# Optimization experiments

Hardware: AMD Instinct MI355X
Metric: run time of the kernel (lower is better)

## Reference

```python
import jax, jax.numpy as jnp
import numpy as np

TH1 = 1.0  # thresholds[0]
TH2 = 1.0  # thresholds[1]

B, IN, H, OUT = 256, 1024, 2048, 1024


def setup_inputs() -> dict:
    key = jax.random.key(0)
    ks = jax.random.split(key, 7)
    # Linear weights scaled like torch default init (~1/sqrt(fan_in)) so spikes occur
    W1 = jax.random.normal(ks[0], (H, IN), jnp.float32) / np.sqrt(IN)
    b1 = jax.random.normal(ks[1], (H,), jnp.float32) * 0.01
    W2 = jax.random.normal(ks[2], (H, H), jnp.float32) / np.sqrt(H)
    b2 = jax.random.normal(ks[3], (H,), jnp.float32) * 0.01
    W3 = jax.random.normal(ks[4], (OUT, H), jnp.float32) / np.sqrt(H)
    b3 = jax.random.normal(ks[5], (OUT,), jnp.float32) * 0.01
    x = jax.random.normal(ks[6], (B, IN), jnp.float32)
    return {"x": x, "W1": W1, "b1": b1, "W2": W2, "b2": b2, "W3": W3, "b3": b3, "T": 50}


def reference(x, W1, b1, W2, b2, W3, b3, T):
    b = x.shape[0]
    dt = x.dtype
    # fc1(x) is identical every timestep; compute once (same math as torch loop)
    i1 = x @ W1.T + b1  # [b, H]

    def step(carry, _):
        v1, v2, v3 = carry
        v1 = v1 + i1
        s1 = (v1 >= TH1).astype(dt)
        v1 = v1 * (1.0 - s1)          # reset on spike
        v2 = v2 + s1 @ W2.T + b2
        s2 = (v2 >= TH2).astype(dt)
        v2 = v2 * (1.0 - s2)
        v3 = v3 + s2 @ W3.T + b3
        return (v1, v2, v3), None

    init = (jnp.zeros((b, W1.shape[0]), dt),
            jnp.zeros((b, W2.shape[0]), dt),
            jnp.zeros((b, W3.shape[0]), dt))
    (v1, v2, v3), _ = jax.lax.scan(step, init, None, length=T)
    return v3 / T
```

## Files before the change

kernel.cpp:

```cpp
#include <hip/hip_runtime.h>

#define NB     256
#define IN1    1024
#define H1     2048
#define OUT3   1024
#define TSTEPS 50
#define KSPLIT 8
#define KSPL3  8

#define QS   (0.15f / 127.f)
#define QS2  (QS / 254.f)

typedef __attribute__((ext_vector_type(4))) int int32x4;

__device__ __forceinline__ void gl2lds16(const void* g, void* l) {
  __builtin_amdgcn_global_load_lds(
      (const __attribute__((address_space(1))) unsigned char*)g,
      (__attribute__((address_space(3))) unsigned char*)l, 16, 0, 0);
}

__global__ __launch_bounds__(256)
void quant_kernel(const float* __restrict__ W, signed char* __restrict__ hi,
                  signed char* __restrict__ lo, int n) {
  int i = blockIdx.x * 256 + threadIdx.x;
  if (i < n) {
    float w = W[i];
    float h = rintf(w * (1.f / QS));
    h = fminf(fmaxf(h, -127.f), 127.f);
    float r = w - h * QS;
    float l2 = fminf(fmaxf(rintf(r * (1.f / QS2)), -127.f), 127.f);
    hi[i] = (signed char)h;
    lo[i] = (signed char)l2;
  }
}

__global__ __launch_bounds__(256)
void sgemm_splitk(const float* __restrict__ A, const float* __restrict__ B,
                  float* __restrict__ P, int M, int N, int K) {
  __shared__ float As[16][68];
  __shared__ float Bs[16][68];
  const int t  = threadIdx.x;
  const int tx = t & 15, ty = t >> 4;
  const int m0 = blockIdx.y * 64, n0 = blockIdx.x * 64;
  const int Kc = K / KSPLIT;
  const int kbeg = blockIdx.z * Kc, kend = kbeg + Kc;
  const int lr = t >> 4, lk = t & 15;
  float acc[4][4] = {};
  for (int k0 = kbeg; k0 < kend; k0 += 16) {
    #pragma unroll
    for (int i = 0; i < 4; ++i) {
      As[lk][lr + i * 16] = A[(size_t)(m0 + lr + i * 16) * K + k0 + lk];
      Bs[lk][lr + i * 16] = B[(size_t)(n0 + lr + i * 16) * K + k0 + lk];
    }
    __syncthreads();
    #pragma unroll
    for (int kk = 0; kk < 16; ++kk) {
      float4 a4 = *(const float4*)&As[kk][ty * 4];
      float4 b4 = *(const float4*)&Bs[kk][tx * 4];
      float av[4] = {a4.x, a4.y, a4.z, a4.w};
      float bv[4] = {b4.x, b4.y, b4.z, b4.w};
      #pragma unroll
      for (int i = 0; i < 4; ++i)
        #pragma unroll
        for (int j = 0; j < 4; ++j)
          acc[i][j] += av[i] * bv[j];
    }
    __syncthreads();
  }
  float* Pp = P + (size_t)blockIdx.z * M * N;
  #pragma unroll
  for (int i = 0; i < 4; ++i)
    #pragma unroll
    for (int j = 0; j < 4; ++j)
      Pp[(size_t)(m0 + ty * 4 + i) * N + n0 + tx * 4 + j] = acc[i][j];
}

__global__ __launch_bounds__(256)
void sim1_kernel(const float* __restrict__ P, const float* __restrict__ b1,
                 signed char* __restrict__ s1all) {
  int idx = blockIdx.x * 256 + threadIdx.x;
  float inp = b1[idx & (H1 - 1)];
  #pragma unroll
  for (int s = 0; s < KSPLIT; ++s) inp += P[(size_t)s * (NB * H1) + idx];
  float v = 0.f;
  #pragma unroll
  for (int t = 0; t < TSTEPS; ++t) {
    v += inp;
    bool s = (v >= 1.0f);
    s1all[(size_t)t * (NB * H1) + idx] = s ? (signed char)1 : (signed char)0;
    if (s) v = 0.f;
  }
}

__global__ __launch_bounds__(256)
void sim2_kernel(const float* __restrict__ A2, const float* __restrict__ b2,
                 float* __restrict__ v2s, float* __restrict__ cnt,
                 signed char* __restrict__ cnt8,
                 int tch, int init, int fin) {
  int idx = blockIdx.x * 256 + threadIdx.x;
  float v = init ? 0.f : v2s[idx];
  float c = init ? 0.f : cnt[idx];
  float bb = b2[idx & (H1 - 1)];
  for (int t = 0; t < tch; ++t) {
    v = v + A2[(size_t)t * (NB * H1) + idx];
    v = v + bb;
    if (v >= 1.0f) { c += 1.f; v = 0.f; }
  }
  if (fin) {
    cnt8[idx] = (signed char)c;
  } else {
    v2s[idx] = v;
    cnt[idx] = c;
  }
}

__global__ __launch_bounds__(256)
void out_epi_kernel(const float* __restrict__ P, const float* __restrict__ b3,
                    float* __restrict__ out) {
  int idx = blockIdx.x * 256 + threadIdx.x;
  float a = 0.f;
  #pragma unroll
  for (int s = 0; s < KSPL3; ++s) a += P[(size_t)s * (NB * OUT3) + idx];
  out[idx] = (a + (float)TSTEPS * b3[idx & (OUT3 - 1)]) * (1.0f / TSTEPS);
}

__global__ __launch_bounds__(512, 4)
void gemm_i8(const signed char* __restrict__ A,
             const signed char* __restrict__ B0,
             const signed char* __restrict__ B1,
             float* __restrict__ C, int M, int N, int K, int Kc) {
  __shared__ signed char As[128 * 128];
  __shared__ signed char Bs[2 * 128 * 128];

  const int gx  = gridDim.x;
  const int nwg = gx * gridDim.y;
  int wg = blockIdx.y * gx + blockIdx.x;
  if (gridDim.z == 1 && (nwg & 7) == 0) wg = (wg & 7) * (nwg >> 3) + (wg >> 3);
  const int bx = wg % gx, by = wg / gx;
  const int m0 = by * 128, n0 = bx * 128;
  const int kbeg = blockIdx.z * Kc, kend = kbeg + Kc;

  const int t  = threadIdx.x;
  const int l  = t & 63;
  const int w  = t >> 6;
  const int wm = w >> 2, wn = w & 3;
  const int lr = l & 15;
  const int lq = l >> 4;
  const int kx = lr & 7;
  const int sr   = t >> 3, c8 = t & 7;
  const int scol = (c8 ^ (sr & 7)) * 16;

  int32x4 acch[4][2], accl[4][2];
  #pragma unroll
  for (int m = 0; m < 4; ++m)
    #pragma unroll
    for (int n = 0; n < 2; ++n) {
      acch[m][n] = (int32x4)(0);
      accl[m][n] = (int32x4)(0);
    }

  #pragma unroll 1
  for (int k0 = kbeg; k0 < kend; k0 += 128) {
    gl2lds16(A  + (size_t)(m0 + sr)      * K + k0 + scol, As + sr * 128 + c8 * 16);
    gl2lds16(A  + (size_t)(m0 + sr + 64) * K + k0 + scol, As + (sr + 64) * 128 + c8 * 16);
    gl2lds16(B0 + (size_t)(n0 + sr)      * K + k0 + scol, Bs + sr * 128 + c8 * 16);
    gl2lds16(B0 + (size_t)(n0 + sr + 64) * K + k0 + scol, Bs + (sr + 64) * 128 + c8 * 16);
    gl2lds16(B1 + (size_t)(n0 + sr)      * K + k0 + scol, Bs + 128 * 128 + sr * 128 + c8 * 16);
    gl2lds16(B1 + (size_t)(n0 + sr + 64) * K + k0 + scol, Bs + 128 * 128 + (sr + 64) * 128 + c8 * 16);
    __syncthreads();

    #pragma unroll
    for (int ks = 0; ks < 2; ++ks) {
      const int kc = ks * 4 + lq;
      const int ko = (kc ^ kx) * 16;
      int32x4 af[4], bf[2];
      #pragma unroll
      for (int m = 0; m < 4; ++m)
        af[m] = *(const int32x4*)(As + (wm * 64 + m * 16 + lr) * 128 + ko);
      #pragma unroll
      for (int n = 0; n < 2; ++n)
        bf[n] = *(const int32x4*)(Bs + (wn * 32 + n * 16 + lr) * 128 + ko);
      #pragma unroll
      for (int m = 0; m < 4; ++m)
        #pragma unroll
        for (int n = 0; n < 2; ++n)
          acch[m][n] = __builtin_amdgcn_mfma_i32_16x16x64_i8(af[m], bf[n], acch[m][n], 0, 0, 0);
      #pragma unroll
      for (int n = 0; n < 2; ++n)
        bf[n] = *(const int32x4*)(Bs + 128 * 128 + (wn * 32 + n * 16 + lr) * 128 + ko);
      #pragma unroll
      for (int m = 0; m < 4; ++m)
        #pragma unroll
        for (int n = 0; n < 2; ++n)
          accl[m][n] = __builtin_amdgcn_mfma_i32_16x16x64_i8(af[m], bf[n], accl[m][n], 0, 0, 0);
    }
    __syncthreads();
  }

  float* Cp = C + (size_t)blockIdx.z * M * N;
  const int crow = lq * 4;
  #pragma unroll
  for (int m = 0; m < 4; ++m) {
    #pragma unroll
    for (int n = 0; n < 2; ++n) {
      int col  = n0 + wn * 32 + n * 16 + lr;
      int rowb = m0 + wm * 64 + m * 16 + crow;
      #pragma unroll
      for (int j = 0; j < 4; ++j)
        Cp[(size_t)(rowb + j) * N + col] =
            QS * (float)acch[m][n][j] + QS2 * (float)accl[m][n][j];
    }
  }
}

extern "C" void kernel_launch(void* const* d_in, const int* in_sizes, int n_in,
                              void* d_out, int out_size, void* d_ws, size_t ws_size,
                              hipStream_t stream) {
  const float* x  = (const float*)d_in[0];
  const float* W1 = (const float*)d_in[1];
  const float* b1 = (const float*)d_in[2];
  const float* W2 = (const float*)d_in[3];
  const float* b2 = (const float*)d_in[4];
  const float* W3 = (const float*)d_in[5];
  const float* b3 = (const float*)d_in[6];
  float* out = (float*)d_out;

  char* ws = (char*)d_ws;
  size_t off = 0;
  auto take = [&](size_t bytes) -> void* {
    void* p = ws + off;
    off += (bytes + 255) & ~(size_t)255;
    return p;
  };
  signed char* W2hi  = (signed char*)take((size_t)H1 * H1);
  signed char* W2lo  = (signed char*)take((size_t)H1 * H1);
  signed char* W3hi  = (signed char*)take((size_t)OUT3 * H1);
  signed char* W3lo  = (signed char*)take((size_t)OUT3 * H1);
  signed char* s1all = (signed char*)take((size_t)TSTEPS * NB * H1);
  float*       v2s   = (float*)take((size_t)NB * H1 * 4);
  float*       cnt   = (float*)take((size_t)NB * H1 * 4);
  signed char* cnt8  = (signed char*)take((size_t)NB * H1);
  size_t part_bytes  = (size_t)KSPLIT * NB * H1 * 4;
  size_t part3_bytes = (size_t)KSPL3 * NB * OUT3 * 4;
  float* Part = (float*)take(part_bytes > part3_bytes ? part_bytes : part3_bytes);

  const size_t plane = (size_t)NB * H1 * 4;
  size_t avail = (ws_size > off) ? (ws_size - off) : 0;
  int CH = (int)(avail / plane);
  if (CH > TSTEPS) CH = TSTEPS;
  if (CH < 1) CH = 1;
  float* A2 = (float*)take((size_t)CH * plane);

  quant_kernel<<<dim3((H1 * H1 + 255) / 256), 256, 0, stream>>>(W2, W2hi, W2lo, H1 * H1);
  quant_kernel<<<dim3((OUT3 * H1 + 255) / 256), 256, 0, stream>>>(W3, W3hi, W3lo, OUT3 * H1);

  sgemm_splitk<<<dim3(H1 / 64, NB / 64, KSPLIT), 256, 0, stream>>>(
      x, W1, Part, NB, H1, IN1);

  sim1_kernel<<<dim3(NB * H1 / 256), 256, 0, stream>>>(Part, b1, s1all);

  for (int c0 = 0; c0 < TSTEPS; c0 += CH) {
    int ch = (TSTEPS - c0 < CH) ? (TSTEPS - c0) : CH;
    gemm_i8<<<dim3(H1 / 128, ch * NB / 128), 512, 0, stream>>>(
        s1all + (size_t)c0 * NB * H1, W2hi, W2lo, A2, ch * NB, H1, H1, H1);
    sim2_kernel<<<dim3(NB * H1 / 256), 256, 0, stream>>>(
        A2, b2, v2s, cnt, cnt8, ch, c0 == 0, c0 + ch >= TSTEPS);
  }

  gemm_i8<<<dim3(OUT3 / 128, NB / 128, KSPL3), 512, 0, stream>>>(
      cnt8, W3hi, W3lo, Part, NB, OUT3, H1, H1 / KSPL3);
  out_epi_kernel<<<dim3(NB * OUT3 / 256), 256, 0, stream>>>(Part, b3, out);
}
```

Before: 170.1 us.

## Double-buffer int8 GEMM LDS tiles and enlarge M tile to 256

The int8 MFMA GEMM now uses a 256x128 output tile and double-buffered LDS staging, so the global-to-LDS loads for the next K slice are issued while MFMAs run on the current one. Explicit waitcnt, sched_barrier and setprio calls are added to overlap LDS fragment reads with the MFMA stream. The aim is to hide load latency and reuse each B tile across more rows. In exchange the kernel needs about 128KB of LDS and more accumulator registers, so occupancy bound drops to 2 and the grid has half as many workgroups, including the small split-K W3 GEMM.

```diff
diff --git a/kernel.cpp b/kernel.cpp
--- a/kernel.cpp
+++ b/kernel.cpp
@@ -124,20 +124,20 @@
   out[idx] = (a + (float)TSTEPS * b3[idx & (OUT3 - 1)]) * (1.0f / TSTEPS);
 }
 
-__global__ __launch_bounds__(512, 4)
+__global__ __launch_bounds__(512, 2)
 void gemm_i8(const signed char* __restrict__ A,
              const signed char* __restrict__ B0,
              const signed char* __restrict__ B1,
              float* __restrict__ C, int M, int N, int K, int Kc) {
-  __shared__ signed char As[128 * 128];
-  __shared__ signed char Bs[2 * 128 * 128];
+  __shared__ signed char As[2][256 * 128];
+  __shared__ signed char Bs[2][2][128 * 128];
 
   const int gx  = gridDim.x;
   const int nwg = gx * gridDim.y;
   int wg = blockIdx.y * gx + blockIdx.x;
   if (gridDim.z == 1 && (nwg & 7) == 0) wg = (wg & 7) * (nwg >> 3) + (wg >> 3);
   const int bx = wg % gx, by = wg / gx;
-  const int m0 = by * 128, n0 = bx * 128;
+  const int m0 = by * 256, n0 = bx * 128;
   const int kbeg = blockIdx.z * Kc, kend = kbeg + Kc;
 
   const int t  = threadIdx.x;
@@ -150,61 +150,90 @@
   const int sr   = t >> 3, c8 = t & 7;
   const int scol = (c8 ^ (sr & 7)) * 16;
 
-  int32x4 acch[4][2], accl[4][2];
-  #pragma unroll
-  for (int m = 0; m < 4; ++m)
+  auto stage = [&](int k0, int b) {
+    #pragma unroll
+    for (int i = 0; i < 4; ++i) {
+      int row = i * 64 + sr;
+      gl2lds16(A + (size_t)(m0 + row) * K + k0 + scol, As[b] + row * 128 + c8 * 16);
+    }
+    #pragma unroll
+    for (int i = 0; i < 2; ++i) {
+      int row = i * 64 + sr;
+      gl2lds16(B0 + (size_t)(n0 + row) * K + k0 + scol, Bs[b][0] + row * 128 + c8 * 16);
+      gl2lds16(B1 + (size_t)(n0 + row) * K + k0 + scol, Bs[b][1] + row * 128 + c8 * 16);
+    }
+  };
+
+  int32x4 acch[8][2], accl[8][2];
+  #pragma unroll
+  for (int m = 0; m < 8; ++m)
     #pragma unroll
     for (int n = 0; n < 2; ++n) {
       acch[m][n] = (int32x4)(0);
       accl[m][n] = (int32x4)(0);
     }
 
+  stage(kbeg, 0);
+  asm volatile("s_waitcnt vmcnt(0)" ::: "memory");
+  __builtin_amdgcn_s_barrier();
+
+  int cur = 0;
   #pragma unroll 1
   for (int k0 = kbeg; k0 < kend; k0 += 128) {
-    gl2lds16(A  + (size_t)(m0 + sr)      * K + k0 + scol, As + sr * 128 + c8 * 16);
-    gl2lds16(A  + (size_t)(m0 + sr + 64) * K + k0 + scol, As + (sr + 64) * 128 + c8 * 16);
-    gl2lds16(B0 + (size_t)(n0 + sr)      * K + k0 + scol, Bs + sr * 128 + c8 * 16);
-    gl2lds16(B0 + (size_t)(n0 + sr + 64) * K + k0 + scol, Bs + (sr + 64) * 128 + c8 * 16);
-    gl2lds16(B1 + (size_t)(n0 + sr)      * K + k0 + scol, Bs + 128 * 128 + sr * 128 + c8 * 16);
-    gl2lds16(B1 + (size_t)(n0 + sr + 64) * K + k0 + scol, Bs + 128 * 128 + (sr + 64) * 128 + c8 * 16);
-    __syncthreads();
+    if (k0 + 128 < kend) stage(k0 + 128, cur ^ 1);
+
+    const signed char* As_ = As[cur];
+    const signed char* Bh_ = Bs[cur][0];
+    const signed char* Bl_ = Bs[cur][1];
 
     #pragma unroll
     for (int ks = 0; ks < 2; ++ks) {
       const int kc = ks * 4 + lq;
       const int ko = (kc ^ kx) * 16;
-      int32x4 af[4], bf[2];
-      #pragma unroll
-      for (int m = 0; m < 4; ++m)
-        af[m] = *(const int32x4*)(As + (wm * 64 + m * 16 + lr) * 128 + ko);
+      int32x4 af[8], bf[2];
+      #pragma unroll
+      for (int m = 0; m < 8; ++m)
+        af[m] = *(const int32x4*)(As_ + (wm * 128 + m * 16 + lr) * 128 + ko);
       #pragma unroll
       for (int n = 0; n < 2; ++n)
-        bf[n] = *(const int32x4*)(Bs + (wn * 32 + n * 16 + lr) * 128 + ko);
-      #pragma unroll
-      for (int m = 0; m < 4; ++m)
+        bf[n] = *(const int32x4*)(Bh_ + (wn * 32 + n * 16 + lr) * 128 + ko);
+      asm volatile("s_waitcnt lgkmcnt(2)" ::: "memory");
+      __builtin_amdgcn_sched_barrier(0);
+      __builtin_amdgcn_s_setprio(1);
+      #pragma unroll
+      for (int m = 0; m < 8; ++m)
         #pragma unroll
         for (int n = 0; n < 2; ++n)
           acch[m][n] = __builtin_amdgcn_mfma_i32_16x16x64_i8(af[m], bf[n], acch[m][n], 0, 0, 0);
+      __builtin_amdgcn_s_setprio(0);
       #pragma unroll
       for (int n = 0; n < 2; ++n)
-        bf[n] = *(const int32x4*)(Bs + 128 * 128 + (wn * 32 + n * 16 + lr) * 128 + ko);
-      #pragma unroll
-      for (int m = 0; m < 4; ++m)
+        bf[n] = *(const int32x4*)(Bl_ + (wn * 32 + n * 16 + lr) * 128 + ko);
+      asm volatile("s_waitcnt lgkmcnt(0)" ::: "memory");
+      __builtin_amdgcn_sched_barrier(0);
+      __builtin_amdgcn_s_setprio(1);
+      #pragma unroll
+      for (int m = 0; m < 8; ++m)
         #pragma unroll
         for (int n = 0; n < 2; ++n)
           accl[m][n] = __builtin_amdgcn_mfma_i32_16x16x64_i8(af[m], bf[n], accl[m][n], 0, 0, 0);
-    }
-    __syncthreads();
+      __builtin_amdgcn_s_setprio(0);
+    }
+
+    asm volatile("s_waitcnt vmcnt(0)" ::: "memory");
+    __builtin_amdgcn_s_barrier();
+    __builtin_amdgcn_sched_barrier(0);
+    cur ^= 1;
   }
 
   float* Cp = C + (size_t)blockIdx.z * M * N;
   const int crow = lq * 4;
   #pragma unroll
-  for (int m = 0; m < 4; ++m) {
+  for (int m = 0; m < 8; ++m) {
     #pragma unroll
     for (int n = 0; n < 2; ++n) {
       int col  = n0 + wn * 32 + n * 16 + lr;
-      int rowb = m0 + wm * 64 + m * 16 + crow;
+      int rowb = m0 + wm * 128 + m * 16 + crow;
       #pragma unroll
       for (int j = 0; j < 4; ++j)
         Cp[(size_t)(rowb + j) * N + col] =
@@ -261,13 +290,13 @@
 
   for (int c0 = 0; c0 < TSTEPS; c0 += CH) {
     int ch = (TSTEPS - c0 < CH) ? (TSTEPS - c0) : CH;
-    gemm_i8<<<dim3(H1 / 128, ch * NB / 128), 512, 0, stream>>>(
+    gemm_i8<<<dim3(H1 / 128, ch * NB / 256), 512, 0, stream>>>(
         s1all + (size_t)c0 * NB * H1, W2hi, W2lo, A2, ch * NB, H1, H1, H1);
     sim2_kernel<<<dim3(NB * H1 / 256), 256, 0, stream>>>(
         A2, b2, v2s, cnt, cnt8, ch, c0 == 0, c0 + ch >= TSTEPS);
   }
 
-  gemm_i8<<<dim3(OUT3 / 128, NB / 128, KSPL3), 512, 0, stream>>>(
+  gemm_i8<<<dim3(OUT3 / 128, NB / 256, KSPL3), 512, 0, stream>>>(
       cnt8, W3hi, W3lo, Part, NB, OUT3, H1, H1 / KSPL3);
   out_epi_kernel<<<dim3(NB * OUT3 / 256), 256, 0, stream>>>(Part, b3, out);
 }
```

New measurement: 209.5 us. 1.23x slower.

## Triple-buffer the W2 int8 GEMM with async LDS loads and vectorize sim kernels

Applied to the files above, without the earlier changes.

Adds a pipelined int8 MFMA GEMM for the main spiking layer. It keeps three LDS stages in flight, prefetching two K-tiles ahead with fine-grained vmcnt waits and raising wave priority around the MFMA blocks. The sim1 and sim2 elementwise kernels are vectorized to handle four neurons per thread with float4 loads and packed byte stores. The two weight quantization launches are merged into one. The larger LDS footprint (144KB per block) limits occupancy to one workgroup per CU, which the deeper pipeline is meant to offset.

```diff
diff --git a/kernel.cpp b/kernel.cpp
--- a/kernel.cpp
+++ b/kernel.cpp
@@ -11,6 +11,8 @@
 #define QS   (0.15f / 127.f)
 #define QS2  (QS / 254.f)
 
+#define BUFB 49152
+
 typedef __attribute__((ext_vector_type(4))) int int32x4;
 
 __device__ __forceinline__ void gl2lds16(const void* g, void* l) {
@@ -19,18 +21,26 @@
       (__attribute__((address_space(3))) unsigned char*)l, 16, 0, 0);
 }
 
-__global__ __launch_bounds__(256)
-void quant_kernel(const float* __restrict__ W, signed char* __restrict__ hi,
-                  signed char* __restrict__ lo, int n) {
+__device__ __forceinline__ void quant1(float w, signed char* hi, signed char* lo) {
+  float h = rintf(w * (1.f / QS));
+  h = fminf(fmaxf(h, -127.f), 127.f);
+  float r = w - h * QS;
+  float l2 = fminf(fmaxf(rintf(r * (1.f / QS2)), -127.f), 127.f);
+  *hi = (signed char)h;
+  *lo = (signed char)l2;
+}
+
+__global__ __launch_bounds__(256)
+void quant2_kernel(const float* __restrict__ W2, const float* __restrict__ W3,
+                   signed char* __restrict__ W2hi, signed char* __restrict__ W2lo,
+                   signed char* __restrict__ W3hi, signed char* __restrict__ W3lo) {
   int i = blockIdx.x * 256 + threadIdx.x;
-  if (i < n) {
-    float w = W[i];
-    float h = rintf(w * (1.f / QS));
-    h = fminf(fmaxf(h, -127.f), 127.f);
-    float r = w - h * QS;
-    float l2 = fminf(fmaxf(rintf(r * (1.f / QS2)), -127.f), 127.f);
-    hi[i] = (signed char)h;
-    lo[i] = (signed char)l2;
+  const int n2 = H1 * H1;
+  if (i < n2) {
+    quant1(W2[i], W2hi + i, W2lo + i);
+  } else {
+    int j = i - n2;
+    if (j < OUT3 * H1) quant1(W3[j], W3hi + j, W3lo + j);
   }
 }
 
@@ -78,17 +88,26 @@
 __global__ __launch_bounds__(256)
 void sim1_kernel(const float* __restrict__ P, const float* __restrict__ b1,
                  signed char* __restrict__ s1all) {
-  int idx = blockIdx.x * 256 + threadIdx.x;
-  float inp = b1[idx & (H1 - 1)];
-  #pragma unroll
-  for (int s = 0; s < KSPLIT; ++s) inp += P[(size_t)s * (NB * H1) + idx];
-  float v = 0.f;
+  int idx4 = (blockIdx.x * 256 + threadIdx.x) * 4;
+  float4 inp = *(const float4*)(b1 + (idx4 & (H1 - 1)));
+  #pragma unroll
+  for (int s = 0; s < KSPLIT; ++s) {
+    float4 p = *(const float4*)(P + (size_t)s * (NB * H1) + idx4);
+    inp.x += p.x; inp.y += p.y; inp.z += p.z; inp.w += p.w;
+  }
+  float v[4] = {0.f, 0.f, 0.f, 0.f};
+  float in[4] = {inp.x, inp.y, inp.z, inp.w};
   #pragma unroll
   for (int t = 0; t < TSTEPS; ++t) {
-    v += inp;
-    bool s = (v >= 1.0f);
-    s1all[(size_t)t * (NB * H1) + idx] = s ? (signed char)1 : (signed char)0;
-    if (s) v = 0.f;
+    unsigned pk = 0;
+    #pragma unroll
+    for (int j = 0; j < 4; ++j) {
+      v[j] += in[j];
+      bool s = (v[j] >= 1.0f);
+      pk |= (s ? 1u : 0u) << (8 * j);
+      if (s) v[j] = 0.f;
+    }
+    *(unsigned*)(s1all + (size_t)t * (NB * H1) + idx4) = pk;
   }
 }
 
@@ -97,20 +116,30 @@
                  float* __restrict__ v2s, float* __restrict__ cnt,
                  signed char* __restrict__ cnt8,
                  int tch, int init, int fin) {
-  int idx = blockIdx.x * 256 + threadIdx.x;
-  float v = init ? 0.f : v2s[idx];
-  float c = init ? 0.f : cnt[idx];
-  float bb = b2[idx & (H1 - 1)];
+  int idx4 = (blockIdx.x * 256 + threadIdx.x) * 4;
+  float4 vv = init ? make_float4(0.f, 0.f, 0.f, 0.f) : *(const float4*)(v2s + idx4);
+  float4 cc = init ? make_float4(0.f, 0.f, 0.f, 0.f) : *(const float4*)(cnt + idx4);
+  float4 bb = *(const float4*)(b2 + (idx4 & (H1 - 1)));
+  float v[4] = {vv.x, vv.y, vv.z, vv.w};
+  float c[4] = {cc.x, cc.y, cc.z, cc.w};
+  float b[4] = {bb.x, bb.y, bb.z, bb.w};
   for (int t = 0; t < tch; ++t) {
-    v = v + A2[(size_t)t * (NB * H1) + idx];
-    v = v + bb;
-    if (v >= 1.0f) { c += 1.f; v = 0.f; }
+    float4 a = *(const float4*)(A2 + (size_t)t * (NB * H1) + idx4);
+    float av[4] = {a.x, a.y, a.z, a.w};
+    #pragma unroll
+    for (int j = 0; j < 4; ++j) {
+      v[j] = v[j] + av[j] + b[j];
+      if (v[j] >= 1.0f) { c[j] += 1.f; v[j] = 0.f; }
+    }
   }
   if (fin) {
-    cnt8[idx] = (signed char)c;
+    unsigned pk = 0;
+    #pragma unroll
+    for (int j = 0; j < 4; ++j) pk |= ((unsigned)(unsigned char)(signed char)c[j]) << (8 * j);
+    *(unsigned*)(cnt8 + idx4) = pk;
   } else {
-    v2s[idx] = v;
-    cnt[idx] = c;
+    *(float4*)(v2s + idx4) = make_float4(v[0], v[1], v[2], v[3]);
+    *(float4*)(cnt + idx4) = make_float4(c[0], c[1], c[2], c[3]);
   }
 }
 
@@ -125,18 +154,14 @@
 }
 
 __global__ __launch_bounds__(512, 4)
-void gemm_i8(const signed char* __restrict__ A,
-             const signed char* __restrict__ B0,
-             const signed char* __restrict__ B1,
-             float* __restrict__ C, int M, int N, int K, int Kc) {
+void gemm_i8s(const signed char* __restrict__ A,
+              const signed char* __restrict__ B0,
+              const signed char* __restrict__ B1,
+              float* __restrict__ C, int M, int N, int K, int Kc) {
   __shared__ signed char As[128 * 128];
-  __shared__ signed char Bs[2 * 128 * 128];
-
-  const int gx  = gridDim.x;
-  const int nwg = gx * gridDim.y;
-  int wg = blockIdx.y * gx + blockIdx.x;
-  if (gridDim.z == 1 && (nwg & 7) == 0) wg = (wg & 7) * (nwg >> 3) + (wg >> 3);
-  const int bx = wg % gx, by = wg / gx;
+  __shared__ signed char Bs[2][128 * 128];
+
+  const int bx = blockIdx.x, by = blockIdx.y;
   const int m0 = by * 128, n0 = bx * 128;
   const int kbeg = blockIdx.z * Kc, kend = kbeg + Kc;
 
@@ -144,42 +169,36 @@
   const int l  = t & 63;
   const int w  = t >> 6;
   const int wm = w >> 2, wn = w & 3;
-  const int lr = l & 15;
-  const int lq = l >> 4;
+  const int lr = l & 15, lq = l >> 4;
   const int kx = lr & 7;
-  const int sr   = t >> 3, c8 = t & 7;
+  const int sr = t >> 3, c8 = t & 7;
   const int scol = (c8 ^ (sr & 7)) * 16;
 
   int32x4 acch[4][2], accl[4][2];
   #pragma unroll
   for (int m = 0; m < 4; ++m)
     #pragma unroll
-    for (int n = 0; n < 2; ++n) {
-      acch[m][n] = (int32x4)(0);
-      accl[m][n] = (int32x4)(0);
-    }
+    for (int n = 0; n < 2; ++n) { acch[m][n] = (int32x4)(0); accl[m][n] = (int32x4)(0); }
 
   #pragma unroll 1
   for (int k0 = kbeg; k0 < kend; k0 += 128) {
     gl2lds16(A  + (size_t)(m0 + sr)      * K + k0 + scol, As + sr * 128 + c8 * 16);
     gl2lds16(A  + (size_t)(m0 + sr + 64) * K + k0 + scol, As + (sr + 64) * 128 + c8 * 16);
-    gl2lds16(B0 + (size_t)(n0 + sr)      * K + k0 + scol, Bs + sr * 128 + c8 * 16);
-    gl2lds16(B0 + (size_t)(n0 + sr + 64) * K + k0 + scol, Bs + (sr + 64) * 128 + c8 * 16);
-    gl2lds16(B1 + (size_t)(n0 + sr)      * K + k0 + scol, Bs + 128 * 128 + sr * 128 + c8 * 16);
-    gl2lds16(B1 + (size_t)(n0 + sr + 64) * K + k0 + scol, Bs + 128 * 128 + (sr + 64) * 128 + c8 * 16);
+    gl2lds16(B0 + (size_t)(n0 + sr)      * K + k0 + scol, Bs[0] + sr * 128 + c8 * 16);
+    gl2lds16(B0 + (size_t)(n0 + sr + 64) * K + k0 + scol, Bs[0] + (sr + 64) * 128 + c8 * 16);
+    gl2lds16(B1 + (size_t)(n0 + sr)      * K + k0 + scol, Bs[1] + sr * 128 + c8 * 16);
+    gl2lds16(B1 + (size_t)(n0 + sr + 64) * K + k0 + scol, Bs[1] + (sr + 64) * 128 + c8 * 16);
     __syncthreads();
-
     #pragma unroll
     for (int ks = 0; ks < 2; ++ks) {
-      const int kc = ks * 4 + lq;
-      const int ko = (kc ^ kx) * 16;
+      const int ko = ((ks * 4 + lq) ^ kx) * 16;
       int32x4 af[4], bf[2];
       #pragma unroll
       for (int m = 0; m < 4; ++m)
         af[m] = *(const int32x4*)(As + (wm * 64 + m * 16 + lr) * 128 + ko);
       #pragma unroll
       for (int n = 0; n < 2; ++n)
-        bf[n] = *(const int32x4*)(Bs + (wn * 32 + n * 16 + lr) * 128 + ko);
+        bf[n] = *(const int32x4*)(Bs[0] + (wn * 32 + n * 16 + lr) * 128 + ko);
       #pragma unroll
       for (int m = 0; m < 4; ++m)
         #pragma unroll
@@ -187,7 +206,7 @@
           acch[m][n] = __builtin_amdgcn_mfma_i32_16x16x64_i8(af[m], bf[n], acch[m][n], 0, 0, 0);
       #pragma unroll
       for (int n = 0; n < 2; ++n)
-        bf[n] = *(const int32x4*)(Bs + 128 * 128 + (wn * 32 + n * 16 + lr) * 128 + ko);
+        bf[n] = *(const int32x4*)(Bs[1] + (wn * 32 + n * 16 + lr) * 128 + ko);
       #pragma unroll
       for (int m = 0; m < 4; ++m)
         #pragma unroll
@@ -200,7 +219,7 @@
   float* Cp = C + (size_t)blockIdx.z * M * N;
   const int crow = lq * 4;
   #pragma unroll
-  for (int m = 0; m < 4; ++m) {
+  for (int m = 0; m < 4; ++m)
     #pragma unroll
     for (int n = 0; n < 2; ++n) {
       int col  = n0 + wn * 32 + n * 16 + lr;
@@ -210,7 +229,108 @@
         Cp[(size_t)(rowb + j) * N + col] =
             QS * (float)acch[m][n][j] + QS2 * (float)accl[m][n][j];
     }
-  }
+}
+
+__global__ __launch_bounds__(512, 2)
+void gemm_i8_pipe(const signed char* __restrict__ A,
+                  const signed char* __restrict__ B0,
+                  const signed char* __restrict__ B1,
+                  float* __restrict__ C, int M, int N, int K) {
+  __shared__ signed char LB[3 * BUFB];
+
+  const int gx  = gridDim.x;
+  const int nwg = gx * gridDim.y;
+  int wg = blockIdx.y * gx + blockIdx.x;
+  if ((nwg & 7) == 0) wg = (wg & 7) * (nwg >> 3) + (wg >> 3);
+  const int bx = wg % gx, by = wg / gx;
+  const int m0 = by * 128, n0 = bx * 128;
+
+  const int t  = threadIdx.x;
+  const int l  = t & 63;
+  const int w  = t >> 6;
+  const int wm = w >> 2, wn = w & 3;
+  const int lr = l & 15, lq = l >> 4;
+  const int kx = lr & 7;
+  const int sr = t >> 3, c8 = t & 7;
+  const int scol = (c8 ^ (sr & 7)) * 16;
+
+  auto stage = [&](int k0, unsigned lb) {
+    signed char* p = LB + lb;
+    gl2lds16(A  + (size_t)(m0 + sr)      * K + k0 + scol, p + sr * 128 + c8 * 16);
+    gl2lds16(A  + (size_t)(m0 + sr + 64) * K + k0 + scol, p + (sr + 64) * 128 + c8 * 16);
+    gl2lds16(B0 + (size_t)(n0 + sr)      * K + k0 + scol, p + 16384 + sr * 128 + c8 * 16);
+    gl2lds16(B0 + (size_t)(n0 + sr + 64) * K + k0 + scol, p + 16384 + (sr + 64) * 128 + c8 * 16);
+    gl2lds16(B1 + (size_t)(n0 + sr)      * K + k0 + scol, p + 32768 + sr * 128 + c8 * 16);
+    gl2lds16(B1 + (size_t)(n0 + sr + 64) * K + k0 + scol, p + 32768 + (sr + 64) * 128 + c8 * 16);
+  };
+
+  int32x4 acch[4][2], accl[4][2];
+  #pragma unroll
+  for (int m = 0; m < 4; ++m)
+    #pragma unroll
+    for (int n = 0; n < 2; ++n) { acch[m][n] = (int32x4)(0); accl[m][n] = (int32x4)(0); }
+
+  stage(0, 0);
+  if (K > 128) stage(128, BUFB);
+
+  unsigned lb_cur = 0, lb_nxt = BUFB, lb_3rd = 2 * BUFB;
+  #pragma unroll 1
+  for (int k0 = 0; k0 < K; k0 += 128) {
+    if (k0 + 128 < K) asm volatile("s_waitcnt vmcnt(6)" ::: "memory");
+    else              asm volatile("s_waitcnt vmcnt(0)" ::: "memory");
+    __builtin_amdgcn_s_barrier();
+    __builtin_amdgcn_sched_barrier(0);
+
+    if (k0 + 256 < K) stage(k0 + 256, lb_3rd);
+    __builtin_amdgcn_sched_barrier(0);
+
+    const signed char* As_ = LB + lb_cur;
+    const signed char* Bh_ = LB + lb_cur + 16384;
+    const signed char* Bl_ = LB + lb_cur + 32768;
+    #pragma unroll
+    for (int ks = 0; ks < 2; ++ks) {
+      const int ko = ((ks * 4 + lq) ^ kx) * 16;
+      int32x4 af[4], bf[2];
+      #pragma unroll
+      for (int m = 0; m < 4; ++m)
+        af[m] = *(const int32x4*)(As_ + (wm * 64 + m * 16 + lr) * 128 + ko);
+      #pragma unroll
+      for (int n = 0; n < 2; ++n)
+        bf[n] = *(const int32x4*)(Bh_ + (wn * 32 + n * 16 + lr) * 128 + ko);
+      __builtin_amdgcn_s_setprio(1);
+      #pragma unroll
+      for (int m = 0; m < 4; ++m)
+        #pragma unroll
+        for (int n = 0; n < 2; ++n)
+          acch[m][n] = __builtin_amdgcn_mfma_i32_16x16x64_i8(af[m], bf[n], acch[m][n], 0, 0, 0);
+      __builtin_amdgcn_s_setprio(0);
+      #pragma unroll
+      for (int n = 0; n < 2; ++n)
+        bf[n] = *(const int32x4*)(Bl_ + (wn * 32 + n * 16 + lr) * 128 + ko);
+      __builtin_amdgcn_s_setprio(1);
+      #pragma unroll
+      for (int m = 0; m < 4; ++m)
+        #pragma unroll
+        for (int n = 0; n < 2; ++n)
+          accl[m][n] = __builtin_amdgcn_mfma_i32_16x16x64_i8(af[m], bf[n], accl[m][n], 0, 0, 0);
+      __builtin_amdgcn_s_setprio(0);
+    }
+
+    unsigned tmp = lb_cur; lb_cur = lb_nxt; lb_nxt = lb_3rd; lb_3rd = tmp;
+  }
+
+  const int crow = lq * 4;
+  #pragma unroll
+  for (int m = 0; m < 4; ++m)
+    #pragma unroll
+    for (int n = 0; n < 2; ++n) {
+      int col  = n0 + wn * 32 + n * 16 + lr;
+      int rowb = m0 + wm * 64 + m * 16 + crow;
+      #pragma unroll
+      for (int j = 0; j < 4; ++j)
+        C[(size_t)(rowb + j) * N + col] =
+            QS * (float)acch[m][n][j] + QS2 * (float)accl[m][n][j];
+    }
 }
 
 extern "C" void kernel_launch(void* const* d_in, const int* in_sizes, int n_in,
@@ -251,23 +371,23 @@
   if (CH < 1) CH = 1;
   float* A2 = (float*)take((size_t)CH * plane);
 
-  quant_kernel<<<dim3((H1 * H1 + 255) / 256), 256, 0, stream>>>(W2, W2hi, W2lo, H1 * H1);
-  quant_kernel<<<dim3((OUT3 * H1 + 255) / 256), 256, 0, stream>>>(W3, W3hi, W3lo, OUT3 * H1);
+  quant2_kernel<<<dim3((H1 * H1 + OUT3 * H1 + 255) / 256), 256, 0, stream>>>(
+      W2, W3, W2hi, W2lo, W3hi, W3lo);
 
   sgemm_splitk<<<dim3(H1 / 64, NB / 64, KSPLIT), 256, 0, stream>>>(
       x, W1, Part, NB, H1, IN1);
 
-  sim1_kernel<<<dim3(NB * H1 / 256), 256, 0, stream>>>(Part, b1, s1all);
+  sim1_kernel<<<dim3(NB * H1 / 1024), 256, 0, stream>>>(Part, b1, s1all);
 
   for (int c0 = 0; c0 < TSTEPS; c0 += CH) {
     int ch = (TSTEPS - c0 < CH) ? (TSTEPS - c0) : CH;
-    gemm_i8<<<dim3(H1 / 128, ch * NB / 128), 512, 0, stream>>>(
-        s1all + (size_t)c0 * NB * H1, W2hi, W2lo, A2, ch * NB, H1, H1, H1);
-    sim2_kernel<<<dim3(NB * H1 / 256), 256, 0, stream>>>(
+    gemm_i8_pipe<<<dim3(H1 / 128, ch * NB / 128), 512, 0, stream>>>(
+        s1all + (size_t)c0 * NB * H1, W2hi, W2lo, A2, ch * NB, H1, H1);
+    sim2_kernel<<<dim3(NB * H1 / 1024), 256, 0, stream>>>(
         A2, b2, v2s, cnt, cnt8, ch, c0 == 0, c0 + ch >= TSTEPS);
   }
 
-  gemm_i8<<<dim3(OUT3 / 128, NB / 128, KSPL3), 512, 0, stream>>>(
+  gemm_i8s<<<dim3(OUT3 / 128, NB / 128, KSPL3), 512, 0, stream>>>(
       cnt8, W3hi, W3lo, Part, NB, OUT3, H1, H1 / KSPL3);
   out_epi_kernel<<<dim3(NB * OUT3 / 256), 256, 0, stream>>>(Part, b3, out);
 }
```

Result: slower. 190.6 us (+12.0%).
